# Performance work log

Measured on AMD Instinct MI355X. Metric: run time of the kernel, lower is better.

The kernel has to match this reference:

```python
import jax, jax.numpy as jnp
import numpy as np

B, S, D, H = 2, 2048, 1024, 16
HD = D // H          # 64
HALF = HD // 2       # 32
EPS = 1e-6           # RMSNorm eps (module default eps=1e-6)


def setup_inputs() -> dict:
    key = jax.random.key(0)
    ks = jax.random.split(key, 6)
    x = jax.random.normal(ks[0], (B, S, D), jnp.float32)
    scale = 1.0 / np.sqrt(D)
    Wq = jax.random.normal(ks[1], (D, D), jnp.float32) * scale
    Wk = jax.random.normal(ks[2], (D, D), jnp.float32) * scale
    Wv = jax.random.normal(ks[3], (D, D), jnp.float32) * scale
    Wo = jax.random.normal(ks[4], (D, D), jnp.float32) * scale
    bq = jnp.zeros((D,), jnp.float32)
    bk = jnp.zeros((D,), jnp.float32)
    bv = jnp.zeros((D,), jnp.float32)
    bo = jnp.zeros((D,), jnp.float32)
    gq = jnp.ones((D,), jnp.float32)   # norm_q weight
    gk = jnp.ones((D,), jnp.float32)   # norm_k weight
    # Standard RoPE angles: pos * 10000^(-2i/head_dim); freqs = exp(i*ang)
    pos = jnp.arange(S, dtype=jnp.float32)
    inv_freq = 1.0 / (10000.0 ** (jnp.arange(0, HD, 2, dtype=jnp.float32) / HD))
    ang = pos[:, None] * inv_freq[None, :]          # (S, HALF)
    return dict(x=x, Wq=Wq, bq=bq, Wk=Wk, bk=bk, Wv=Wv, bv=bv, Wo=Wo, bo=bo,
                gq=gq, gk=gk, freqs_cos=jnp.cos(ang), freqs_sin=jnp.sin(ang))


def _rmsnorm(x, g):
    # x * rsqrt(mean(x^2) + eps) * g, computed in fp32 as in the torch module
    return x * jax.lax.rsqrt(jnp.mean(x * x, axis=-1, keepdims=True) + EPS) * g


def _rope(x, cos, sin):
    # x: (B,S,D) packed heads; rotate consecutive (even,odd) pairs per head.
    xr = x.reshape(B, S, H, HALF, 2)
    x0, x1 = xr[..., 0], xr[..., 1]
    c = cos[None, :, None, :]  # (1,S,1,HALF)
    s = sin[None, :, None, :]
    o0 = x0 * c - x1 * s
    o1 = x0 * s + x1 * c
    return jnp.stack([o0, o1], axis=-1).reshape(B, S, D)


def reference(x, Wq, bq, Wk, bk, Wv, bv, Wo, bo, gq, gk, freqs_cos, freqs_sin):
    q = _rmsnorm(x @ Wq.T + bq, gq)
    k = _rmsnorm(x @ Wk.T + bk, gk)
    v = x @ Wv.T + bv
    q = _rope(q, freqs_cos, freqs_sin)
    k = _rope(k, freqs_cos, freqs_sin)
    # SDPA (non-causal, as F.scaled_dot_product_attention default call)
    qh = q.reshape(B, S, H, HD)
    kh = k.reshape(B, S, H, HD)
    vh = v.reshape(B, S, H, HD)
    scores = jnp.einsum('bqhd,bkhd->bhqk', qh, kh) / np.sqrt(HD)
    attn = jax.nn.softmax(scores, axis=-1)
    out = jnp.einsum('bhqk,bkhd->bqhd', attn, vh).reshape(B, S, D)
    return out @ Wo.T + bo
```

## Files before the change

kernel.cpp:

```cpp
#include <hip/hip_runtime.h>

typedef unsigned short u16;
typedef unsigned int u32;
typedef u16 u16x4 __attribute__((ext_vector_type(4)));
typedef u16 u16x8 __attribute__((ext_vector_type(8)));
typedef u32 u32x4 __attribute__((ext_vector_type(4)));
typedef float f32x4 __attribute__((ext_vector_type(4)));
typedef float f32x16 __attribute__((ext_vector_type(16)));
typedef __bf16 bf16x2 __attribute__((ext_vector_type(2)));
typedef __bf16 bf16x8 __attribute__((ext_vector_type(8)));

#define GLOAD16(gp, lp)                                             \
  __builtin_amdgcn_global_load_lds(                                 \
      (const __attribute__((address_space(1))) void*)(gp),          \
      (__attribute__((address_space(3))) void*)(lp), 16, 0, 0)

__device__ __forceinline__ u16 f2bf(float f) {
  unsigned int u = __builtin_bit_cast(unsigned int, f);
  u += 0x7FFFu + ((u >> 16) & 1u);
  return (u16)(u >> 16);
}
__device__ __forceinline__ float bf2f(u16 h) {
  return __builtin_bit_cast(float, (u32)h << 16);
}

__global__ __launch_bounds__(256) void f2b_kernel(const float* __restrict__ in,
                                                  u16* __restrict__ out, int n4) {
  int i = blockIdx.x * 256 + threadIdx.x;
  if (i < n4) {
    f32x4 v = *(const f32x4*)(in + (size_t)i * 4);
    u16x4 o;
    o[0] = f2bf(v[0]); o[1] = f2bf(v[1]); o[2] = f2bf(v[2]); o[3] = f2bf(v[3]);
    *(u16x4*)(out + (size_t)i * 4) = o;
  }
}

__global__ __launch_bounds__(256) void f2bw_kernel(const float* __restrict__ s0,
    const float* __restrict__ s1, const float* __restrict__ s2,
    const float* __restrict__ s3, u16* __restrict__ dst) {
  const int y = blockIdx.y;
  const float* s = (y == 0) ? s0 : ((y == 1) ? s1 : ((y == 2) ? s2 : s3));
  int i = blockIdx.x * 256 + threadIdx.x;
  f32x4 v = *(const f32x4*)(s + (size_t)i * 4);
  u16x4 o;
  o[0] = f2bf(v[0]); o[1] = f2bf(v[1]); o[2] = f2bf(v[2]); o[3] = f2bf(v[3]);
  *(u16x4*)(dst + (size_t)y * 1048576 + (size_t)i * 4) = o;
}

__device__ __forceinline__ void gemm_core(const u16* __restrict__ A,
                                          const u16* __restrict__ W,
                                          int bm0, int bn0,
                                          u16* ldsA, u16* ldsB,
                                          f32x4 acc[4][4]) {
  const int tid = threadIdx.x;
  const int l = tid & 63;
  const int lr = l & 15, lk = l >> 4;
  const int w = tid >> 6;
  const int wr = w >> 1, wc = w & 1;
  const int srow = tid >> 2, sko = (tid & 3) << 3;
  auto stage = [&](int kt, int buf) {
#pragma unroll
    for (int it = 0; it < 2; ++it) {
      int row = it * 64 + srow;
      GLOAD16(A + (size_t)(bm0 + row) * 1024 + kt * 32 + sko,
              ldsA + buf * 4096 + (it * 256 + tid) * 8);
      GLOAD16(W + (size_t)(bn0 + row) * 1024 + kt * 32 + sko,
              ldsB + buf * 4096 + (it * 256 + tid) * 8);
    }
  };
  stage(0, 0);
  stage(1, 1);
  int cur = 0, nx2 = 2;
  for (int kt = 0; kt < 32; ++kt) {
    if (kt < 31) asm volatile("s_waitcnt vmcnt(4)" ::: "memory");
    else         asm volatile("s_waitcnt vmcnt(0)" ::: "memory");
    __builtin_amdgcn_s_barrier();
    __builtin_amdgcn_sched_barrier(0);
    if (kt + 2 < 32) stage(kt + 2, nx2);
    const u16* lA = ldsA + cur * 4096;
    const u16* lB = ldsB + cur * 4096;
    bf16x8 af[4], bfr[4];
#pragma unroll
    for (int m = 0; m < 4; ++m)
      af[m] = *(const bf16x8*)(lA + (wr * 64 + m * 16 + lr) * 32 + lk * 8);
#pragma unroll
    for (int n = 0; n < 4; ++n)
      bfr[n] = *(const bf16x8*)(lB + (wc * 64 + n * 16 + lr) * 32 + lk * 8);
#pragma unroll
    for (int m = 0; m < 4; ++m)
#pragma unroll
      for (int n = 0; n < 4; ++n)
        acc[m][n] = __builtin_amdgcn_mfma_f32_16x16x32_bf16(af[m], bfr[n], acc[m][n], 0, 0, 0);
    cur = (cur == 2) ? 0 : cur + 1;
    nx2 = (nx2 == 2) ? 0 : nx2 + 1;
  }
}

__global__ __launch_bounds__(256) void qkv_gemm(const u16* __restrict__ xb,
    const u16* __restrict__ wq, const u16* __restrict__ wk, const u16* __restrict__ wv,
    const float* __restrict__ bq, const float* __restrict__ bk, const float* __restrict__ bv,
    u16* __restrict__ Qb, u16* __restrict__ Kb, u16* __restrict__ Vf) {
  __shared__ u16 ldsA[3 * 4096];
  __shared__ u16 ldsB[3 * 4096];
  const int z = blockIdx.z;
  const u16* W = (z == 0) ? wq : ((z == 1) ? wk : wv);
  const float* bias = (z == 0) ? bq : ((z == 1) ? bk : bv);
  const int bm0 = blockIdx.x * 128, bn0 = blockIdx.y * 128;
  const f32x4 zf = {0.f, 0.f, 0.f, 0.f};
  f32x4 acc[4][4];
#pragma unroll
  for (int m = 0; m < 4; ++m)
#pragma unroll
    for (int n = 0; n < 4; ++n) acc[m][n] = zf;
  gemm_core(xb, W, bm0, bn0, ldsA, ldsB, acc);
  const int tid = threadIdx.x, l = tid & 63, lr = l & 15, lk = l >> 4;
  const int w = tid >> 6, wr = w >> 1, wc = w & 1;
  float bcol[4];
#pragma unroll
  for (int n = 0; n < 4; ++n) bcol[n] = bias[bn0 + wc * 64 + n * 16 + lr];
  if (z < 2) {
    u16* outp = z ? Kb : Qb;
#pragma unroll
    for (int m = 0; m < 4; ++m)
#pragma unroll
      for (int n = 0; n < 4; ++n)
#pragma unroll
        for (int r = 0; r < 4; ++r) {
          int row = bm0 + wr * 64 + m * 16 + lk * 4 + r;
          int col = bn0 + wc * 64 + n * 16 + lr;
          outp[(size_t)row * 1024 + col] = f2bf(acc[m][n][r] + bcol[n]);
        }
  } else {
#pragma unroll
    for (int m = 0; m < 4; ++m)
#pragma unroll
      for (int n = 0; n < 4; ++n) {
        int row = bm0 + wr * 64 + m * 16 + lk * 4;
        int col = bn0 + wc * 64 + n * 16 + lr;
        int b = row >> 11, sf = row & 2047, hh = col >> 6, hd = col & 63;
        int t = sf >> 6, kin = sf & 63;
        int ks = kin >> 4, hiv = (kin >> 3) & 1, j0 = kin & 7;
        int vhalf = hd >> 5, lq = hd & 31;
        u16x4 o;
#pragma unroll
        for (int r = 0; r < 4; ++r) o[r] = f2bf(acc[m][n][r] + bcol[n]);
        size_t addr = (size_t)(b * 16 + hh) * 131072 +
                      (size_t)(((t * 4 + ks) * 2 + vhalf)) * 512 +
                      ((hiv << 5) + lq) * 8 + j0;
        *(u16x4*)(Vf + addr) = o;
      }
  }
}

__global__ __launch_bounds__(256) void proj_gemm(const u16* __restrict__ ctx,
    const u16* __restrict__ wo, const float* __restrict__ bo, float* __restrict__ out) {
  __shared__ u16 ldsA[3 * 4096];
  __shared__ u16 ldsB[3 * 4096];
  const int bm0 = blockIdx.x * 128, bn0 = blockIdx.y * 128;
  const f32x4 zf = {0.f, 0.f, 0.f, 0.f};
  f32x4 acc[4][4];
#pragma unroll
  for (int m = 0; m < 4; ++m)
#pragma unroll
    for (int n = 0; n < 4; ++n) acc[m][n] = zf;
  gemm_core(ctx, wo, bm0, bn0, ldsA, ldsB, acc);
  const int tid = threadIdx.x, l = tid & 63, lr = l & 15, lk = l >> 4;
  const int w = tid >> 6, wr = w >> 1, wc = w & 1;
  float bcol[4];
#pragma unroll
  for (int n = 0; n < 4; ++n) bcol[n] = bo[bn0 + wc * 64 + n * 16 + lr];
#pragma unroll
  for (int m = 0; m < 4; ++m)
#pragma unroll
    for (int n = 0; n < 4; ++n)
#pragma unroll
      for (int r = 0; r < 4; ++r) {
        int row = bm0 + wr * 64 + m * 16 + lk * 4 + r;
        int col = bn0 + wc * 64 + n * 16 + lr;
        out[(size_t)row * 1024 + col] = acc[m][n][r] + bcol[n];
      }
}

__global__ __launch_bounds__(256) void rmsrope(const u16* __restrict__ Qb,
    const u16* __restrict__ Kb, const float* __restrict__ gq, const float* __restrict__ gk,
    const float* __restrict__ fc, const float* __restrict__ fs,
    u16* __restrict__ Qf, u16* __restrict__ Kf) {
  const int row = blockIdx.x;
  const int which = blockIdx.y;
  const u16* src = (which ? Kb : Qb) + (size_t)row * 1024;
  const float* g = which ? gk : gq;
  const int t = threadIdx.x;
  u16x4 raw = *(const u16x4*)(src + t * 4);
  float v0 = bf2f(raw[0]), v1 = bf2f(raw[1]), v2 = bf2f(raw[2]), v3 = bf2f(raw[3]);
  float ss = v0 * v0 + v1 * v1 + v2 * v2 + v3 * v3;
#pragma unroll
  for (int mm = 1; mm < 64; mm <<= 1) ss += __shfl_xor(ss, mm);
  __shared__ float red[4];
  if ((t & 63) == 0) red[t >> 6] = ss;
  __syncthreads();
  float rstd = rsqrtf((red[0] + red[1] + red[2] + red[3]) * (1.0f / 1024.0f) + 1e-6f);
  if (!which) rstd *= 0.18033688011112042f;
  int d = t * 4, hh = d >> 6, dh = d & 63, p = dh >> 1;
  int s = row & 2047, b = row >> 11;
  float c0 = fc[(s << 5) + p], s0 = fs[(s << 5) + p];
  float c1 = fc[(s << 5) + p + 1], s1 = fs[(s << 5) + p + 1];
  float x0 = v0 * rstd * g[d];
  float x1 = v1 * rstd * g[d + 1];
  float x2 = v2 * rstd * g[d + 2];
  float x3 = v3 * rstd * g[d + 3];
  u16x4 o;
  o[0] = f2bf(x0 * c0 - x1 * s0);
  o[1] = f2bf(x0 * s0 + x1 * c0);
  o[2] = f2bf(x2 * c1 - x3 * s1);
  o[3] = f2bf(x2 * s1 + x3 * c1);
  const size_t base = (size_t)(b * 16 + hh) * 131072;
  const int hs = dh >> 4, hi = (dh >> 3) & 1, j0 = dh & 7;
  size_t addr;
  if (!which) {
    addr = base + (size_t)((s >> 5) * 4 + hs) * 512 + ((hi << 5) + (s & 31)) * 8 + j0;
  } else {
    addr = base + (size_t)(((s >> 6) * 4 + hs) * 2 + ((s >> 5) & 1)) * 512 +
           ((hi << 5) + (s & 31)) * 8 + j0;
  }
  *(u16x4*)((which ? Kf : Qf) + addr) = o;
}

__global__ __launch_bounds__(256) void attn_kernel(const u16* __restrict__ Qf,
    const u16* __restrict__ Kf, const u16* __restrict__ Vf, u16* __restrict__ ctx) {
  const int tid = threadIdx.x;
  const int w = tid >> 6, l = tid & 63;
  const int lq = l & 31, hi = l >> 5;
  const bool hiB = (hi != 0);
  const int id = blockIdx.x;
  const int qt = (id >> 3) & 15;
  const int hb = (id & 7) | ((id >> 7) << 3);
  const int h = hb & 15, b = hb >> 4;
  const int bh = b * 16 + h;
  const u16* Qp = Qf + (size_t)bh * 131072;
  const u16* Kp = Kf + (size_t)bh * 131072;
  const u16* Vp = Vf + (size_t)bh * 131072;
  bf16x8 qf[4];
#pragma unroll
  for (int hs = 0; hs < 4; ++hs)
    qf[hs] = *(const bf16x8*)(Qp + (size_t)((qt * 4 + w) * 4 + hs) * 512 + l * 8);

  auto ldK = [&](int t, bf16x8* kr) {
#pragma unroll
    for (int i = 0; i < 8; ++i)
      kr[i] = *(const bf16x8*)(Kp + ((size_t)t * 8 + i) * 512 + l * 8);
  };
  auto ldV = [&](int t, bf16x8* vr) {
#pragma unroll
    for (int i = 0; i < 8; ++i)
      vr[i] = *(const bf16x8*)(Vp + ((size_t)t * 8 + i) * 512 + l * 8);
  };

  const f32x16 z16 = {0,0,0,0, 0,0,0,0, 0,0,0,0, 0,0,0,0};
  f32x16 O0 = z16, O1 = z16;
  float lsum = 0.f;

  auto qk_step = [&](const bf16x8* kr, f32x16& s0, f32x16& s1) {
    s0 = z16; s1 = z16;
    __builtin_amdgcn_s_setprio(1);
#pragma unroll
    for (int hs = 0; hs < 4; ++hs) {
      s0 = __builtin_amdgcn_mfma_f32_32x32x16_bf16(kr[hs * 2 + 0], qf[hs], s0, 0, 0, 0);
      s1 = __builtin_amdgcn_mfma_f32_32x32x16_bf16(kr[hs * 2 + 1], qf[hs], s1, 0, 0, 0);
    }
    __builtin_amdgcn_s_setprio(0);
  };

  auto sm_pv = [&](const bf16x8* vr, f32x16& sc0, f32x16& sc1) {
    float rs = 0.f;
    u32 pk0[8], pk1[8];
#pragma unroll
    for (int m = 0; m < 8; ++m) {
      float a0 = __builtin_amdgcn_exp2f(sc0[2 * m]);
      float a1 = __builtin_amdgcn_exp2f(sc0[2 * m + 1]);
      float c0 = __builtin_amdgcn_exp2f(sc1[2 * m]);
      float c1 = __builtin_amdgcn_exp2f(sc1[2 * m + 1]);
      rs += (a0 + a1) + (c0 + c1);
      bf16x2 pA; pA[0] = (__bf16)a0; pA[1] = (__bf16)a1;
      bf16x2 pC; pC[0] = (__bf16)c0; pC[1] = (__bf16)c1;
      pk0[m] = __builtin_bit_cast(u32, pA);
      pk1[m] = __builtin_bit_cast(u32, pC);
    }
    rs += __shfl_xor(rs, 32);
    lsum += rs;
    auto xchg = [&](u32 X, u32 Y, u32& wlo, u32& whi) {
      u32 s1v = hiB ? X : Y;
      u32 r = (u32)__shfl_xor((int)s1v, 32);
      wlo = hiB ? r : X;
      whi = hiB ? Y : r;
    };
    bf16x8 pb[4];
    {
      u32 w0, w1, w2, w3;
      xchg(pk0[0], pk0[2], w0, w2);
      xchg(pk0[1], pk0[3], w1, w3);
      u32x4 pw = {w0, w1, w2, w3};
      pb[0] = __builtin_bit_cast(bf16x8, pw);
      xchg(pk0[4], pk0[6], w0, w2);
      xchg(pk0[5], pk0[7], w1, w3);
      u32x4 pw1 = {w0, w1, w2, w3};
      pb[1] = __builtin_bit_cast(bf16x8, pw1);
      xchg(pk1[0], pk1[2], w0, w2);
      xchg(pk1[1], pk1[3], w1, w3);
      u32x4 pw2 = {w0, w1, w2, w3};
      pb[2] = __builtin_bit_cast(bf16x8, pw2);
      xchg(pk1[4], pk1[6], w0, w2);
      xchg(pk1[5], pk1[7], w1, w3);
      u32x4 pw3 = {w0, w1, w2, w3};
      pb[3] = __builtin_bit_cast(bf16x8, pw3);
    }
    __builtin_amdgcn_s_setprio(1);
#pragma unroll
    for (int ks = 0; ks < 4; ++ks) {
      O0 = __builtin_amdgcn_mfma_f32_32x32x16_bf16(vr[ks * 2 + 0], pb[ks], O0, 0, 0, 0);
      O1 = __builtin_amdgcn_mfma_f32_32x32x16_bf16(vr[ks * 2 + 1], pb[ks], O1, 0, 0, 0);
    }
    __builtin_amdgcn_s_setprio(0);
  };

  bf16x8 kE[8], kO[8], vE[8], vO[8];
  f32x16 scA0, scA1, scB0, scB1;
  ldK(0, kE);
  ldV(0, vE);
  ldK(1, kO);
  qk_step(kE, scA0, scA1);
#pragma unroll 1
  for (int dt = 0; dt < 16; ++dt) {
    const int t = dt * 2;
    {
      if (t + 2 < 32) ldK(t + 2, kE);
      ldV(t + 1, vO);
      qk_step(kO, scB0, scB1);
      sm_pv(vE, scA0, scA1);
    }
    {
      if (t + 3 < 32) ldK(t + 3, kO);
      if (t + 2 < 32) {
        ldV(t + 2, vE);
        qk_step(kE, scA0, scA1);
      }
      sm_pv(vO, scB0, scB1);
    }
  }
  float inv = 1.0f / lsum;
  const int q0 = qt * 128 + w * 32;
  const size_t rowoff = ((size_t)(b * 2048 + q0 + lq)) * 1024 + h * 64;
#pragma unroll
  for (int g = 0; g < 4; ++g) {
    u16x4 oa, ob;
#pragma unroll
    for (int rr = 0; rr < 4; ++rr) {
      oa[rr] = f2bf(O0[4 * g + rr] * inv);
      ob[rr] = f2bf(O1[4 * g + rr] * inv);
    }
    *(u16x4*)(ctx + rowoff + 8 * g + 4 * hi) = oa;
    *(u16x4*)(ctx + rowoff + 32 + 8 * g + 4 * hi) = ob;
  }
}

extern "C" void kernel_launch(void* const* d_in, const int* in_sizes, int n_in,
                              void* d_out, int out_size, void* d_ws, size_t ws_size,
                              hipStream_t stream) {
  (void)in_sizes; (void)n_in; (void)out_size; (void)ws_size;
  const float* x  = (const float*)d_in[0];
  const float* Wq = (const float*)d_in[1];
  const float* bq = (const float*)d_in[2];
  const float* Wk = (const float*)d_in[3];
  const float* bk = (const float*)d_in[4];
  const float* Wv = (const float*)d_in[5];
  const float* bv = (const float*)d_in[6];
  const float* Wo = (const float*)d_in[7];
  const float* bo = (const float*)d_in[8];
  const float* gq = (const float*)d_in[9];
  const float* gk = (const float*)d_in[10];
  const float* fc = (const float*)d_in[11];
  const float* fs = (const float*)d_in[12];
  float* out = (float*)d_out;
  char* ws = (char*)d_ws;
  u16*  xb  = (u16*)(ws + 0);
  u16*  wqb = (u16*)(ws + 8388608);
  u16*  wkb = (u16*)(ws + 10485760);
  u16*  wvb = (u16*)(ws + 12582912);
  u16*  wob = (u16*)(ws + 14680064);
  u16*  Qfb = (u16*)(ws + 16777216);
  u16*  Kfb = (u16*)(ws + 25165824);
  u16*  Qfr = (u16*)(ws + 33554432);
  u16*  Kfr = (u16*)(ws + 41943040);
  u16*  Vfr = (u16*)(ws + 50331648);
  u16*  ctx = (u16*)(ws + 58720256);

  f2b_kernel<<<4096, 256, 0, stream>>>(x, xb, 1048576);
  f2bw_kernel<<<dim3(1024, 4), 256, 0, stream>>>(Wq, Wk, Wv, Wo, wqb);
  qkv_gemm<<<dim3(32, 8, 3), 256, 0, stream>>>(xb, wqb, wkb, wvb, bq, bk, bv, Qfb, Kfb, Vfr);
  rmsrope<<<dim3(4096, 2), 256, 0, stream>>>(Qfb, Kfb, gq, gk, fc, fs, Qfr, Kfr);
  attn_kernel<<<512, 256, 0, stream>>>(Qfr, Kfr, Vfr, ctx);
  proj_gemm<<<dim3(32, 8), 256, 0, stream>>>(ctx, wob, bo, out);
}
```

Before: 143.5 us.

## Share K tiles through LDS in attention and merge fp32-to-bf16 conversion kernels

Each attention block now loads each K tile once into a triple-buffered LDS ring with direct global-to-LDS loads, and all four waves read it from there. Before, every wave loaded K into its own registers. The loop is simplified from a two-tile software pipeline to one tile per step with a waitcnt and a barrier. This cuts redundant global K traffic and register pressure, but adds a per-iteration barrier and loses the QK/softmax overlap across tiles. Separately, the x and weight conversion kernels are merged into a single launch.

```diff
diff --git a/kernel.cpp b/kernel.cpp
--- a/kernel.cpp
+++ b/kernel.cpp
@@ -24,27 +24,28 @@
   return __builtin_bit_cast(float, (u32)h << 16);
 }
 
-__global__ __launch_bounds__(256) void f2b_kernel(const float* __restrict__ in,
-                                                  u16* __restrict__ out, int n4) {
-  int i = blockIdx.x * 256 + threadIdx.x;
-  if (i < n4) {
-    f32x4 v = *(const f32x4*)(in + (size_t)i * 4);
-    u16x4 o;
-    o[0] = f2bf(v[0]); o[1] = f2bf(v[1]); o[2] = f2bf(v[2]); o[3] = f2bf(v[3]);
-    *(u16x4*)(out + (size_t)i * 4) = o;
-  }
-}
-
-__global__ __launch_bounds__(256) void f2bw_kernel(const float* __restrict__ s0,
-    const float* __restrict__ s1, const float* __restrict__ s2,
-    const float* __restrict__ s3, u16* __restrict__ dst) {
-  const int y = blockIdx.y;
-  const float* s = (y == 0) ? s0 : ((y == 1) ? s1 : ((y == 2) ? s2 : s3));
-  int i = blockIdx.x * 256 + threadIdx.x;
-  f32x4 v = *(const f32x4*)(s + (size_t)i * 4);
+__global__ __launch_bounds__(256) void f2ball_kernel(const float* __restrict__ x,
+    const float* __restrict__ w0, const float* __restrict__ w1,
+    const float* __restrict__ w2, const float* __restrict__ w3,
+    u16* __restrict__ xb, u16* __restrict__ wb) {
+  int g = blockIdx.x * 256 + threadIdx.x;
+  const float* s;
+  u16* d;
+  size_t off;
+  if (g < 1048576) {
+    s = x; d = xb; off = (size_t)g * 4;
+  } else {
+    int wi = g - 1048576;
+    int sel = wi >> 18;
+    int r = wi & 262143;
+    s = (sel == 0) ? w0 : ((sel == 1) ? w1 : ((sel == 2) ? w2 : w3));
+    d = wb + (size_t)sel * 1048576;
+    off = (size_t)r * 4;
+  }
+  f32x4 v = *(const f32x4*)(s + off);
   u16x4 o;
   o[0] = f2bf(v[0]); o[1] = f2bf(v[1]); o[2] = f2bf(v[2]); o[3] = f2bf(v[3]);
-  *(u16x4*)(dst + (size_t)y * 1048576 + (size_t)i * 4) = o;
+  *(u16x4*)(d + off) = o;
 }
 
 __device__ __forceinline__ void gemm_core(const u16* __restrict__ A,
@@ -227,6 +228,7 @@
 
 __global__ __launch_bounds__(256) void attn_kernel(const u16* __restrict__ Qf,
     const u16* __restrict__ Kf, const u16* __restrict__ Vf, u16* __restrict__ ctx) {
+  __shared__ u16 Kbuf[3][4096];
   const int tid = threadIdx.x;
   const int w = tid >> 6, l = tid & 63;
   const int lq = l & 31, hi = l >> 5;
@@ -244,10 +246,9 @@
   for (int hs = 0; hs < 4; ++hs)
     qf[hs] = *(const bf16x8*)(Qp + (size_t)((qt * 4 + w) * 4 + hs) * 512 + l * 8);
 
-  auto ldK = [&](int t, bf16x8* kr) {
-#pragma unroll
-    for (int i = 0; i < 8; ++i)
-      kr[i] = *(const bf16x8*)(Kp + ((size_t)t * 8 + i) * 512 + l * 8);
+  auto stageK = [&](int t, int buf) {
+    GLOAD16(Kp + (size_t)t * 4096 + tid * 8, &Kbuf[buf][tid * 8]);
+    GLOAD16(Kp + (size_t)t * 4096 + 2048 + tid * 8, &Kbuf[buf][2048 + tid * 8]);
   };
   auto ldV = [&](int t, bf16x8* vr) {
 #pragma unroll
@@ -259,13 +260,15 @@
   f32x16 O0 = z16, O1 = z16;
   float lsum = 0.f;
 
-  auto qk_step = [&](const bf16x8* kr, f32x16& s0, f32x16& s1) {
+  auto qk_lds = [&](const u16* Kb_, f32x16& s0, f32x16& s1) {
     s0 = z16; s1 = z16;
     __builtin_amdgcn_s_setprio(1);
 #pragma unroll
     for (int hs = 0; hs < 4; ++hs) {
-      s0 = __builtin_amdgcn_mfma_f32_32x32x16_bf16(kr[hs * 2 + 0], qf[hs], s0, 0, 0, 0);
-      s1 = __builtin_amdgcn_mfma_f32_32x32x16_bf16(kr[hs * 2 + 1], qf[hs], s1, 0, 0, 0);
+      bf16x8 k0 = *(const bf16x8*)(Kb_ + (hs * 2 + 0) * 512 + l * 8);
+      bf16x8 k1 = *(const bf16x8*)(Kb_ + (hs * 2 + 1) * 512 + l * 8);
+      s0 = __builtin_amdgcn_mfma_f32_32x32x16_bf16(k0, qf[hs], s0, 0, 0, 0);
+      s1 = __builtin_amdgcn_mfma_f32_32x32x16_bf16(k1, qf[hs], s1, 0, 0, 0);
     }
     __builtin_amdgcn_s_setprio(0);
   };
@@ -322,29 +325,23 @@
     __builtin_amdgcn_s_setprio(0);
   };
 
-  bf16x8 kE[8], kO[8], vE[8], vO[8];
-  f32x16 scA0, scA1, scB0, scB1;
-  ldK(0, kE);
-  ldV(0, vE);
-  ldK(1, kO);
-  qk_step(kE, scA0, scA1);
+  bf16x8 vV[8];
+  f32x16 scX0, scX1;
+  stageK(0, 0);
+  stageK(1, 1);
+  int cur = 0, nx2 = 2;
 #pragma unroll 1
-  for (int dt = 0; dt < 16; ++dt) {
-    const int t = dt * 2;
-    {
-      if (t + 2 < 32) ldK(t + 2, kE);
-      ldV(t + 1, vO);
-      qk_step(kO, scB0, scB1);
-      sm_pv(vE, scA0, scA1);
-    }
-    {
-      if (t + 3 < 32) ldK(t + 3, kO);
-      if (t + 2 < 32) {
-        ldV(t + 2, vE);
-        qk_step(kE, scA0, scA1);
-      }
-      sm_pv(vO, scB0, scB1);
-    }
+  for (int t = 0; t < 32; ++t) {
+    if (t < 31) asm volatile("s_waitcnt vmcnt(2)" ::: "memory");
+    else        asm volatile("s_waitcnt vmcnt(0)" ::: "memory");
+    __builtin_amdgcn_s_barrier();
+    __builtin_amdgcn_sched_barrier(0);
+    ldV(t, vV);
+    if (t + 2 < 32) stageK(t + 2, nx2);
+    qk_lds(&Kbuf[cur][0], scX0, scX1);
+    sm_pv(vV, scX0, scX1);
+    cur = (cur == 2) ? 0 : cur + 1;
+    nx2 = (nx2 == 2) ? 0 : nx2 + 1;
   }
   float inv = 1.0f / lsum;
   const int q0 = qt * 128 + w * 32;
@@ -393,8 +390,7 @@
   u16*  Vfr = (u16*)(ws + 50331648);
   u16*  ctx = (u16*)(ws + 58720256);
 
-  f2b_kernel<<<4096, 256, 0, stream>>>(x, xb, 1048576);
-  f2bw_kernel<<<dim3(1024, 4), 256, 0, stream>>>(Wq, Wk, Wv, Wo, wqb);
+  f2ball_kernel<<<8192, 256, 0, stream>>>(x, Wq, Wk, Wv, Wo, xb, wqb);
   qkv_gemm<<<dim3(32, 8, 3), 256, 0, stream>>>(xb, wqb, wkb, wvb, bq, bk, bv, Qfb, Kfb, Vfr);
   rmsrope<<<dim3(4096, 2), 256, 0, stream>>>(Qfb, Kfb, gq, gk, fc, fs, Qfr, Kfr);
   attn_kernel<<<512, 256, 0, stream>>>(Qfr, Kfr, Vfr, ctx);
```

New measurement: 141.2 us. No clear change (-1.6%).
